# Optimization experiments

Hardware: AMD Instinct MI355X
Metric: run time of the kernel (lower is better)

Reference implementation:

```python
import jax, jax.numpy as jnp
from jax import lax
import numpy as np

DN = ('NCHW', 'OIHW', 'NCHW')

def conv2d_same(x, w, b):
    # 5x5, stride 1, pad 2 == SAME
    y = lax.conv_general_dilated(x, w, (1, 1), 'SAME', dimension_numbers=DN)
    return y + b[None, :, None, None]

def setup_inputs() -> dict:
    key = jax.random.key(0)
    ks = jax.random.split(key, 5)
    B, S, D = 8, 2048, 1024
    k55 = 0.2  # ~1/sqrt(25) init scale
    return {
        'x':  jax.random.normal(ks[0], (B, S, D), dtype=jnp.float32),
        'w1': jax.random.normal(ks[1], (1, 1, 5, 5), dtype=jnp.float32) * k55,
        'b1': jnp.zeros((1,), jnp.float32),
        'w2': jax.random.normal(ks[2], (1, 1, 5, 5), dtype=jnp.float32) * k55,
        'b2': jnp.zeros((1,), jnp.float32),
        'w3': jax.random.normal(ks[3], (1, 2, 5, 5), dtype=jnp.float32) * k55,
        'b3': jnp.zeros((1,), jnp.float32),
        'w4': jax.random.normal(ks[4], (1, 1, 5, 5), dtype=jnp.float32) * k55,
        'b4': jnp.zeros((1,), jnp.float32),
    }

def reference(x, w1, b1, w2, b2, w3, b3, w4, b4):
    # x: [b, s, d]
    xT = jnp.swapaxes(x, 1, 2)                              # [b, d, s]
    # self-similarity, softmax over BATCH dim (dim=0, as in original)
    NSSM = jax.nn.softmax(jnp.einsum('bsd,btd->bst', x, x), axis=0)   # [b, s, s]
    conv_x  = conv2d_same(x[:, None],  w1, b1)[:, 0]        # [b, s, d]
    conv_xT = conv2d_same(xT[:, None], w2, b2)[:, 0]        # [b, d, s]
    Attention_map = jax.nn.softmax(jnp.matmul(conv_x, conv_xT), axis=0)  # [b, s, s]
    Moca_map = conv2d_same(jnp.stack([NSSM, Attention_map], axis=1), w3, b3)[:, 0]  # [b, s, s]
    conv_g = conv2d_same(x[:, None], w4, b4)[:, 0]          # [b, s, d]
    Wz = jnp.matmul(Moca_map, conv_g)                       # [b, s, d]
    return Wz + x
```

## Files before the change

### kernel.cpp

```cpp
#include <hip/hip_runtime.h>

#define Bz 8
#define Sz 2048
#define Dz 1024

typedef __attribute__((ext_vector_type(8))) _Float16 f16x8;
typedef __attribute__((ext_vector_type(8))) short short8v;
typedef __attribute__((ext_vector_type(4))) short short4v;
typedef __attribute__((ext_vector_type(4))) float f32x4;

__device__ __forceinline__ short f2h(float f) {
    _Float16 h = (_Float16)f;
    return __builtin_bit_cast(short, h);
}
__device__ __forceinline__ float h2f(short s) {
    return (float)__builtin_bit_cast(_Float16, s);
}
__device__ __forceinline__ void gld16(const void* g, void* l) {
    __builtin_amdgcn_global_load_lds(
        (const __attribute__((address_space(1))) void*)g,
        (__attribute__((address_space(3))) void*)l, 16, 0, 0);
}

__global__ __launch_bounds__(256) void conv3_kernel(
    const float* __restrict__ x,
    const float* __restrict__ w1, const float* __restrict__ b1,
    const float* __restrict__ w2, const float* __restrict__ b2,
    short* __restrict__ x16, short* __restrict__ C1f, short* __restrict__ C2f)
{
    __shared__ float w[50];
    __shared__ float bias[2];
    const size_t SD = (size_t)Sz * Dz;
    int tid = threadIdx.x;
    if (tid < 25) w[tid] = w1[tid];
    else if (tid < 50) w[tid] = w2[tid - 25];
    if (tid == 50) { bias[0] = b1[0]; bias[1] = b2[0]; }
    __syncthreads();

    int d4 = tid * 4;
    int y = blockIdx.y;
    int s = ((y & 7) << 8) | (y >> 3);
    int b = blockIdx.z;
    const float* xb = x + (size_t)b * SD + d4;

    float wv[5][12];
#pragma unroll
    for (int i = 0; i < 5; i++) {
        int ss = s + i - 2;
        int ssc = ss < 0 ? 0 : (ss >= Sz ? Sz - 1 : ss);
        const float* rp = xb + (size_t)ssc * Dz;
        if (d4 > 0) *(float4*)&wv[i][0] = *(const float4*)(rp - 4);
        else { wv[i][0] = wv[i][1] = wv[i][2] = wv[i][3] = 0.f; }
        *(float4*)&wv[i][4] = *(const float4*)rp;
        if (d4 < 1020) *(float4*)&wv[i][8] = *(const float4*)(rp + 4);
        else { wv[i][8] = wv[i][9] = wv[i][10] = wv[i][11] = 0.f; }
        if (ss != ssc) {
#pragma unroll
            for (int q = 0; q < 12; q++) wv[i][q] = 0.f;
        }
    }

    float o1[4] = {}, o2[4] = {};
#pragma unroll
    for (int i = 0; i < 5; i++)
#pragma unroll
        for (int j = 0; j < 5; j++) {
            float c1w = w[i * 5 + j], c2w = w[25 + j * 5 + i];
#pragma unroll
            for (int q = 0; q < 4; q++) {
                float v = wv[i][q + j + 2];
                o1[q] = fmaf(c1w, v, o1[q]);
                o2[q] = fmaf(c2w, v, o2[q]);
            }
        }
    size_t o = (size_t)b * SD + (size_t)s * Dz + d4;
    short4v hx, h1, h2;
#pragma unroll
    for (int q = 0; q < 4; q++) {
        hx[q] = f2h(wv[2][q + 4]);
        h1[q] = f2h(o1[q] + bias[0]);
        h2[q] = f2h(o2[q] + bias[1]);
    }
    *(short4v*)(x16 + o) = hx;
    *(short4v*)(C1f + o) = h1;
    *(short4v*)(C2f + o) = h2;
}

__global__ __launch_bounds__(256) void convT_kernel(
    const float* __restrict__ x, const float* __restrict__ w4,
    const float* __restrict__ b4, short* __restrict__ C4T)
{
    __shared__ float xs[68][73];
    __shared__ short ct[64][72];
    __shared__ float w[25];
    __shared__ float bb;
    const size_t SD = (size_t)Sz * Dz;
    int tid = threadIdx.x;
    if (tid < 25) w[tid] = w4[tid];
    if (tid == 25) bb = b4[0];

    int s0 = blockIdx.x * 64, d0 = blockIdx.y * 64, b = blockIdx.z;
    const float* xb = x + (size_t)b * SD;
    for (int k = tid; k < 68 * 68; k += 256) {
        int r = k / 68, c = k - r * 68;
        int gr = s0 - 2 + r, gc = d0 - 2 + c;
        float v = 0.f;
        if (gr >= 0 && gr < Sz && gc >= 0 && gc < Dz) v = xb[(size_t)gr * Dz + gc];
        xs[r][c] = v;
    }
    __syncthreads();

    int sl = tid & 63, dg = tid >> 6;
    float acc[16];
#pragma unroll
    for (int q = 0; q < 16; q++) acc[q] = bb;
#pragma unroll
    for (int i = 0; i < 5; i++) {
        float row[20];
#pragma unroll
        for (int m = 0; m < 20; m++) row[m] = xs[sl + i][dg * 16 + m];
#pragma unroll
        for (int j = 0; j < 5; j++) {
            float wv = w[i * 5 + j];
#pragma unroll
            for (int q = 0; q < 16; q++) acc[q] = fmaf(wv, row[q + j], acc[q]);
        }
    }
#pragma unroll
    for (int q = 0; q < 16; q++) ct[dg * 16 + q][sl] = f2h(acc[q]);
    __syncthreads();

    int dl = tid >> 2, sc = (tid & 3) * 16;
    f16x8 v0 = *(const f16x8*)&ct[dl][sc];
    f16x8 v1 = *(const f16x8*)&ct[dl][sc + 8];
    short* op = C4T + (size_t)b * SD + (size_t)(d0 + dl) * Sz + s0 + sc;
    *(f16x8*)op = v0;
    *(f16x8*)(op + 8) = v1;
}

__global__ __launch_bounds__(512, 2) void logit8_f16(
    const short* __restrict__ Ag, const short* __restrict__ Bg,
    const short* __restrict__ Aa, const short* __restrict__ Ba,
    short* __restrict__ Qg, short* __restrict__ Qa,
    int rlo, int sq256off, long PS)
{
    __shared__ char lds[131072];

    int flat = blockIdx.x + 8 * (blockIdx.y + 4 * blockIdx.z);
    int nid = (flat & 7) * 64 + (flat >> 3);
    int bx = nid & 7, by = (nid >> 3) & 3, bz = nid >> 5;
    const int map = bz >> 3, bzb = bz & 7;
    if (map == 0) {
        int ntl = bx - sq256off;
        if (ntl >= 0 && ntl < 4 && ntl < by) return;
    }

    const size_t SD = (size_t)Sz * Dz;
    const int K = Dz;
    const short* A = (map ? Aa : Ag) + (size_t)bzb * SD;
    const short* B = (map ? Ba : Bg) + (size_t)bzb * SD;
    short* Q = (map ? Qa : Qg) + (size_t)bzb * PS;

    const int m0 = by * 256, n0 = bx * 256;
    const int t = threadIdx.x;
    const int lane = t & 63;
    const int w = t >> 6;
    const int wm = w >> 2, wn = w & 3;
    const int fr = lane & 15;
    const int kb = lane >> 4;

    const int cc16 = ((t & 7) ^ ((t >> 3) & 7)) * 16;
    const int tr = t >> 3;
    const int bdst = (t >> 8) * 8192 + ((t >> 3) & 31) * 128 + (t & 7) * 16;

    auto STA = [&](int tile, int h) {
        char* base = lds + (tile & 1) * 65536;
#pragma unroll
        for (int j = 0; j < 2; j++) {
            int row = m0 + j * 128 + h * 64 + tr;
            gld16((const char*)A + ((size_t)row * K + tile * 64) * 2 + cc16,
                  base + j * 16384 + h * 8192 + t * 16);
        }
    };
    auto STB = [&](int tile, int h) {
        char* base = lds + (tile & 1) * 65536 + 32768;
#pragma unroll
        for (int j = 0; j < 2; j++) {
            int u = j * 64 + tr;
            int row = n0 + (u >> 5) * 64 + h * 32 + (u & 31);
            gld16((const char*)B + ((size_t)row * K + tile * 64) * 2 + cc16,
                  base + j * 16384 + h * 4096 + bdst);
        }
    };

    int aoff[2], boff[2];
#pragma unroll
    for (int ks = 0; ks < 2; ks++) {
        int slot = ((ks * 4 + kb) ^ (fr & 7)) * 16;
        aoff[ks] = (wm * 128 + fr) * 128 + slot;
        boff[ks] = (wn * 64 + fr) * 128 + slot;
    }

    f16x8 aR[8];
    f16x8 bR[2][4];
    f32x4 acc[8][4];
#pragma unroll
    for (int i = 0; i < 8; i++)
#pragma unroll
        for (int j = 0; j < 4; j++) acc[i][j] = (f32x4){0.f, 0.f, 0.f, 0.f};

    auto LDA = [&](int qa, int d) {
        const char* p = lds + d * 65536 + qa * 8192;
#pragma unroll
        for (int f = 0; f < 4; f++)
#pragma unroll
            for (int ks = 0; ks < 2; ks++)
                aR[f * 2 + ks] = *(const f16x8*)(p + aoff[ks] + f * 2048);
    };
    auto LDB = [&](int qb, int d, int which) {
        const char* p = lds + d * 65536 + 32768 + qb * 4096;
#pragma unroll
        for (int g = 0; g < 2; g++)
#pragma unroll
            for (int ks = 0; ks < 2; ks++)
                bR[which][g * 2 + ks] = *(const f16x8*)(p + boff[ks] + g * 2048);
    };
#define MMQ(qa, qb, which)                                                        \
    __builtin_amdgcn_s_setprio(1);                                                \
    _Pragma("unroll") for (int f = 0; f < 4; f++)                                 \
        _Pragma("unroll") for (int g = 0; g < 2; g++)                             \
            _Pragma("unroll") for (int ks = 0; ks < 2; ks++)                      \
                acc[(qa)*4 + f][(qb)*2 + g] = __builtin_amdgcn_mfma_f32_16x16x32_f16( \
                    aR[f * 2 + ks], bR[which][g * 2 + ks], acc[(qa)*4 + f][(qb)*2 + g], 0, 0, 0); \
    __builtin_amdgcn_s_setprio(0);

#define BAR()  __builtin_amdgcn_s_barrier(); __builtin_amdgcn_sched_barrier(0)
#define WAIT4() asm volatile("s_waitcnt vmcnt(4)" ::: "memory"); __builtin_amdgcn_sched_barrier(0)
#define WAIT0() asm volatile("s_waitcnt vmcnt(0)" ::: "memory"); __builtin_amdgcn_sched_barrier(0)

    STA(0, 0); STB(0, 0); STA(0, 1); STB(0, 1);
    STA(1, 0); STB(1, 0);

    const int NIT = K / 128;
    for (int it = 0; it < NIT - 1; ++it) {
        const int V = 2 * it + 1, W = 2 * it + 2, X = 2 * it + 3;
        WAIT4(); BAR();
        STA(V, 1); LDA(0, 0); LDB(0, 0, 0); MMQ(0, 0, 0);
        BAR();
        STB(V, 1); LDB(1, 0, 1); MMQ(0, 1, 1);
        BAR();
        STA(W, 0); LDA(1, 0); MMQ(1, 0, 0);
        BAR();
        STB(W, 0); MMQ(1, 1, 1);
        WAIT4(); BAR();
        STA(W, 1); LDA(0, 1); LDB(0, 1, 0); MMQ(0, 0, 0);
        BAR();
        STB(W, 1); LDB(1, 1, 1); MMQ(0, 1, 1);
        BAR();
        STA(X, 0); LDA(1, 1); MMQ(1, 0, 0);
        BAR();
        STB(X, 0); MMQ(1, 1, 1);
    }
    {
        const int V = 2 * NIT - 1;
        WAIT4(); BAR();
        STA(V, 1); LDA(0, 0); LDB(0, 0, 0); MMQ(0, 0, 0);
        BAR();
        STB(V, 1); LDB(1, 0, 1); MMQ(0, 1, 1);
        BAR();
        LDA(1, 0); MMQ(1, 0, 0);
        BAR();
        MMQ(1, 1, 1);
        WAIT0(); BAR();
        LDA(0, 1); LDB(0, 1, 0); MMQ(0, 0, 0);
        BAR();
        LDB(1, 1, 1); MMQ(0, 1, 1);
        BAR();
        LDA(1, 1); MMQ(1, 0, 0);
        BAR();
        MMQ(1, 1, 1);
    }
#undef MMQ
#undef BAR
#undef WAIT4
#undef WAIT0

#pragma unroll
    for (int mf = 0; mf < 8; mf++)
#pragma unroll
        for (int nf = 0; nf < 4; nf++) {
            int col = n0 + wn * 64 + nf * 16 + fr;
#pragma unroll
            for (int r = 0; r < 4; r++) {
                int rowg = m0 + wm * 128 + mf * 16 + kb * 4 + r;
                float o = acc[mf][nf][r];
                if (map == 0 && rlo + rowg == col) o -= 1024.f;
                Q[(size_t)rowg * Sz + col] = f2h(o);
            }
        }
}

__global__ __launch_bounds__(512, 2) void wz8_f16(
    const short* __restrict__ M0, const short* __restrict__ M1,
    const short* __restrict__ C4Tm,
    const float* __restrict__ X, float* __restrict__ Out,
    long psM0, long psM1)
{
    __shared__ char lds[131072];

    int flat = blockIdx.x + 4 * (blockIdx.y + 8 * blockIdx.z);
    int nid = (flat & 7) * 32 + (flat >> 3);
    int bx = nid & 3, by = (nid >> 2) & 7, bz = nid >> 5;

    const size_t SD = (size_t)Sz * Dz;
    const int K = Sz;
    const short* A0 = M0 + (size_t)bz * psM0;
    const short* A1 = M1 + (size_t)bz * psM1;
    const short* B = C4Tm + (size_t)bz * SD;
    const float* Src = X + (size_t)bz * SD;
    float* C = Out + (size_t)bz * SD;

    const int m0 = by * 256, n0 = bx * 256;
    const int t = threadIdx.x;
    const int lane = t & 63;
    const int w = t >> 6;
    const int wm = w >> 2, wn = w & 3;
    const int fr = lane & 15;
    const int kb = lane >> 4;

    const int cc16 = ((t & 7) ^ ((t >> 3) & 7)) * 16;
    const int tr = t >> 3;
    const int bdst = (t >> 8) * 8192 + ((t >> 3) & 31) * 128 + (t & 7) * 16;

    auto STA = [&](int tile, int h) {
        char* base = lds + (tile & 1) * 65536;
#pragma unroll
        for (int j = 0; j < 2; j++) {
            int row = m0 + j * 128 + h * 64 + tr;
            const short* src = (row < 1022) ? (A0 + (size_t)row * K)
                                            : (A1 + (size_t)(row - 1022) * K);
            gld16((const char*)src + (size_t)tile * 128 + cc16,
                  base + j * 16384 + h * 8192 + t * 16);
        }
    };
    auto STB = [&](int tile, int h) {
        char* base = lds + (tile & 1) * 65536 + 32768;
#pragma unroll
        for (int j = 0; j < 2; j++) {
            int u = j * 64 + tr;
            int row = n0 + (u >> 5) * 64 + h * 32 + (u & 31);
            gld16((const char*)B + ((size_t)row * K + tile * 64) * 2 + cc16,
                  base + j * 16384 + h * 4096 + bdst);
        }
    };

    int aoff[2], boff[2];
#pragma unroll
    for (int ks = 0; ks < 2; ks++) {
        int slot = ((ks * 4 + kb) ^ (fr & 7)) * 16;
        aoff[ks] = (wm * 128 + fr) * 128 + slot;
        boff[ks] = (wn * 64 + fr) * 128 + slot;
    }

    f16x8 aR[8];
    f16x8 bR[2][4];
    f32x4 acc[8][4];
#pragma unroll
    for (int i = 0; i < 8; i++)
#pragma unroll
        for (int j = 0; j < 4; j++) acc[i][j] = (f32x4){0.f, 0.f, 0.f, 0.f};

    auto LDA = [&](int qa, int d) {
        const char* p = lds + d * 65536 + qa * 8192;
#pragma unroll
        for (int f = 0; f < 4; f++)
#pragma unroll
            for (int ks = 0; ks < 2; ks++)
                aR[f * 2 + ks] = *(const f16x8*)(p + aoff[ks] + f * 2048);
    };
    auto LDB = [&](int qb, int d, int which) {
        const char* p = lds + d * 65536 + 32768 + qb * 4096;
#pragma unroll
        for (int g = 0; g < 2; g++)
#pragma unroll
            for (int ks = 0; ks < 2; ks++)
                bR[which][g * 2 + ks] = *(const f16x8*)(p + boff[ks] + g * 2048);
    };
#define MMQ(qa, qb, which)                                                        \
    __builtin_amdgcn_s_setprio(1);                                                \
    _Pragma("unroll") for (int f = 0; f < 4; f++)                                 \
        _Pragma("unroll") for (int g = 0; g < 2; g++)                             \
            _Pragma("unroll") for (int ks = 0; ks < 2; ks++)                      \
                acc[(qa)*4 + f][(qb)*2 + g] = __builtin_amdgcn_mfma_f32_16x16x32_f16( \
                    aR[f * 2 + ks], bR[which][g * 2 + ks], acc[(qa)*4 + f][(qb)*2 + g], 0, 0, 0); \
    __builtin_amdgcn_s_setprio(0);

#define BAR()  __builtin_amdgcn_s_barrier(); __builtin_amdgcn_sched_barrier(0)
#define WAIT4() asm volatile("s_waitcnt vmcnt(4)" ::: "memory"); __builtin_amdgcn_sched_barrier(0)
#define WAIT0() asm volatile("s_waitcnt vmcnt(0)" ::: "memory"); __builtin_amdgcn_sched_barrier(0)

    STA(0, 0); STB(0, 0); STA(0, 1); STB(0, 1);
    STA(1, 0); STB(1, 0);

    const int NIT = K / 128;
    for (int it = 0; it < NIT - 1; ++it) {
        const int V = 2 * it + 1, W = 2 * it + 2, X2 = 2 * it + 3;
        WAIT4(); BAR();
        STA(V, 1); LDA(0, 0); LDB(0, 0, 0); MMQ(0, 0, 0);
        BAR();
        STB(V, 1); LDB(1, 0, 1); MMQ(0, 1, 1);
        BAR();
        STA(W, 0); LDA(1, 0); MMQ(1, 0, 0);
        BAR();
        STB(W, 0); MMQ(1, 1, 1);
        WAIT4(); BAR();
        STA(W, 1); LDA(0, 1); LDB(0, 1, 0); MMQ(0, 0, 0);
        BAR();
        STB(W, 1); LDB(1, 1, 1); MMQ(0, 1, 1);
        BAR();
        STA(X2, 0); LDA(1, 1); MMQ(1, 0, 0);
        BAR();
        STB(X2, 0); MMQ(1, 1, 1);
    }
    {
        const int V = 2 * NIT - 1;
        WAIT4(); BAR();
        STA(V, 1); LDA(0, 0); LDB(0, 0, 0); MMQ(0, 0, 0);
        BAR();
        STB(V, 1); LDB(1, 0, 1); MMQ(0, 1, 1);
        BAR();
        LDA(1, 0); MMQ(1, 0, 0);
        BAR();
        MMQ(1, 1, 1);
        WAIT0(); BAR();
        LDA(0, 1); LDB(0, 1, 0); MMQ(0, 0, 0);
        BAR();
        LDB(1, 1, 1); MMQ(0, 1, 1);
        BAR();
        LDA(1, 1); MMQ(1, 0, 0);
        BAR();
        MMQ(1, 1, 1);
    }
#undef MMQ
#undef BAR
#undef WAIT4
#undef WAIT0

#pragma unroll
    for (int mf = 0; mf < 8; mf++)
#pragma unroll
        for (int nf = 0; nf < 4; nf++) {
            int col = n0 + wn * 64 + nf * 16 + fr;
#pragma unroll
            for (int r = 0; r < 4; r++) {
                int rowg = m0 + wm * 128 + mf * 16 + kb * 4 + r;
                C[(size_t)rowg * Dz + col] = acc[mf][nf][r] + Src[(size_t)rowg * Dz + col];
            }
        }
}

__global__ __launch_bounds__(256) void mirror_g(
    short* __restrict__ F, int o0, long PS)
{
    __shared__ short ts[128][136];
    int p = blockIdx.x, b = blockIdx.y;
    int mi = 1, base = 0;
    while (p >= base + mi) { base += mi; mi++; }
    int nt = p - base;
    short* Fb = F + (size_t)b * PS;
    int t = threadIdx.x;
    int rr = t >> 1, c0 = (t & 1) * 64;
    const short* src = Fb + (size_t)(nt * 128 + rr) * Sz + o0 + mi * 128 + c0;
#pragma unroll
    for (int j = 0; j < 8; j++)
        *(short8v*)&ts[rr][c0 + j * 8] = *(const short8v*)(src + j * 8);
    __syncthreads();
    short* dst = Fb + (size_t)(mi * 128 + rr) * Sz + o0 + nt * 128 + c0;
#pragma unroll
    for (int j = 0; j < 8; j++) {
        short8v v;
#pragma unroll
        for (int e = 0; e < 8; e++) v[e] = ts[c0 + j * 8 + e][rr];
        *(short8v*)(dst + j * 8) = v;
    }
}

__global__ __launch_bounds__(256) void softmax_ip(
    short* __restrict__ Qg, short* __restrict__ Qa, int nElem, long ps)
{
    int i8 = (blockIdx.x * 256 + threadIdx.x) * 8;
    if (i8 >= nElem) return;
    short* Q = blockIdx.z ? Qa : Qg;

    short8v v[Bz];
    float f[Bz][8];
#pragma unroll
    for (int b = 0; b < Bz; b++) {
        v[b] = *(const short8v*)(Q + i8 + (size_t)b * ps);
#pragma unroll
        for (int e = 0; e < 8; e++) f[b][e] = h2f(v[b][e]);
    }
#pragma unroll
    for (int e = 0; e < 8; e++) {
        float mx = f[0][e];
#pragma unroll
        for (int b = 1; b < Bz; b++) mx = fmaxf(mx, f[b][e]);
        float sum = 0.f;
#pragma unroll
        for (int b = 0; b < Bz; b++) { f[b][e] = __expf(f[b][e] - mx); sum += f[b][e]; }
        float inv = 1.f / sum;
#pragma unroll
        for (int b = 0; b < Bz; b++) v[b][e] = f2h(f[b][e] * inv);
    }
#pragma unroll
    for (int b = 0; b < Bz; b++)
        *(short8v*)(Q + i8 + (size_t)b * ps) = v[b];
}

__global__ __launch_bounds__(256) void slab_copy(
    const short* __restrict__ Fg, const short* __restrict__ Fa,
    short* __restrict__ slab, long PS)
{
    int idx = blockIdx.x * 256 + threadIdx.x;
    int e = idx * 8;
    int map = e >> 16;
    int rem = e & 65535;
    int b = rem >> 13;
    int rem2 = rem & 8191;
    int row = rem2 >> 11;
    int col = rem2 & 2047;
    const short* src = (map ? Fa : Fg) + (size_t)b * PS + (size_t)(1020 + row) * Sz + col;
    *(short8v*)(slab + e) = *(const short8v*)src;
}

__global__ __launch_bounds__(256) void moca_kernel(
    const short* __restrict__ Gs, const short* __restrict__ As,
    const short* __restrict__ slab,
    const float* __restrict__ w3, const float* __restrict__ b3,
    short* __restrict__ Mout,
    int o0, int rlo, int slabLo, long psIn, long psOut)
{
    __shared__ float w[50];
    __shared__ float bb;
    int tid = threadIdx.x;
    if (tid < 50) w[tid] = w3[tid];
    if (tid == 50) bb = b3[0];
    __syncthreads();

    int t8 = tid * 8;
    int so = blockIdx.y, b = blockIdx.z;
    int s = o0 + so;
    const short* Gp = Gs + (size_t)b * psIn;
    const short* Ap = As + (size_t)b * psIn;

    float acc[8];
#pragma unroll
    for (int q = 0; q < 8; q++) acc[q] = bb;

#pragma unroll
    for (int i = 0; i < 5; i++) {
        int sr = s + i - 2;
        if (sr < 0 || sr >= Sz) continue;
        const short *gp, *ap;
        size_t ro;
        if (sr >= rlo) { gp = Gp; ap = Ap; ro = (size_t)(sr - rlo) * Sz; }
        else {
            gp = slab + (size_t)b * 8192;
            ap = slab + 65536 + (size_t)b * 8192;
            ro = (size_t)(sr - slabLo) * Sz;
        }
        float gw[16], aw[16];
#pragma unroll
        for (int g = 0; g < 4; g++) {
            int c0 = t8 - 4 + g * 4;
            if (c0 >= 0 && c0 + 3 < Sz) {
                short4v gv = *(const short4v*)(gp + ro + c0);
                short4v av = *(const short4v*)(ap + ro + c0);
#pragma unroll
                for (int e = 0; e < 4; e++) { gw[g * 4 + e] = h2f(gv[e]); aw[g * 4 + e] = h2f(av[e]); }
            } else {
#pragma unroll
                for (int e = 0; e < 4; e++) { gw[g * 4 + e] = 0.f; aw[g * 4 + e] = 0.f; }
            }
        }
#pragma unroll
        for (int j = 0; j < 5; j++) {
            float wg = w[i * 5 + j], wa = w[25 + i * 5 + j];
#pragma unroll
            for (int q = 0; q < 8; q++)
                acc[q] = fmaf(wg, gw[q + j + 2], fmaf(wa, aw[q + j + 2], acc[q]));
        }
    }
    short4v r0, r1;
#pragma unroll
    for (int q = 0; q < 4; q++) { r0[q] = f2h(acc[q]); r1[q] = f2h(acc[q + 4]); }
    short* op = Mout + (size_t)b * psOut + (size_t)so * Sz + t8;
    *(short4v*)op = r0;
    *(short4v*)(op + 4) = r1;
}

extern "C" void kernel_launch(void* const* d_in, const int* in_sizes, int n_in,
                              void* d_out, int out_size, void* d_ws, size_t ws_size,
                              hipStream_t stream)
{
    const float* x  = (const float*)d_in[0];
    const float* w1 = (const float*)d_in[1];
    const float* b1 = (const float*)d_in[2];
    const float* w2 = (const float*)d_in[3];
    const float* b2 = (const float*)d_in[4];
    const float* w3 = (const float*)d_in[5];
    const float* b3 = (const float*)d_in[6];
    const float* w4 = (const float*)d_in[7];
    const float* b4 = (const float*)d_in[8];
    float* out = (float*)d_out;

    const size_t SD = (size_t)Sz * Dz;
    const size_t BSD2 = (size_t)Bz * SD * 2;

    char* ws = (char*)d_ws;
    short* x16 = (short*)(ws);
    short* C1f = (short*)(ws + 1 * BSD2);
    short* C2f = (short*)(ws + 2 * BSD2);
    short* C4T = (short*)(ws + 3 * BSD2);
    char* strip0 = ws + 4 * BSD2;

    const size_t PS   = (size_t)1024 * Sz;
    const size_t PSM0 = (size_t)1022 * Sz;
    const size_t PSM1 = (size_t)1026 * Sz;
    short* Fg   = (short*)strip0;
    short* Fa   = Fg + (size_t)Bz * PS;
    short* Mf0  = Fa + (size_t)Bz * PS;
    short* slab = Mf0 + (size_t)Bz * PSM0;
    short* Mf1  = x16;

    conv3_kernel<<<dim3(1, Sz, Bz), 256, 0, stream>>>(
        x, w1, b1, w2, b2, x16, C1f, C2f);
    convT_kernel<<<dim3(Sz / 64, Dz / 64, Bz), 256, 0, stream>>>(x, w4, b4, C4T);

    const int ne = 1024 * Sz;

    logit8_f16<<<dim3(8, 4, 16), 512, 0, stream>>>(
        x16, x16, C1f, C2f, Fg, Fa, 0, 0, (long)PS);
    mirror_g<<<dim3(28, Bz), 256, 0, stream>>>(Fg, 0, (long)PS);
    softmax_ip<<<dim3((ne / 8 + 255) / 256, 1, 2), 256, 0, stream>>>(Fg, Fa, ne, (long)PS);
    slab_copy<<<dim3(64), 256, 0, stream>>>(Fg, Fa, slab, (long)PS);
    moca_kernel<<<dim3(1, 1022, Bz), 256, 0, stream>>>(
        Fg, Fa, slab, w3, b3, Mf0, 0, 0, 0, (long)PS, (long)PSM0);

    logit8_f16<<<dim3(8, 4, 16), 512, 0, stream>>>(
        x16 + (size_t)1024 * Dz, x16, C1f + (size_t)1024 * Dz, C2f,
        Fg, Fa, 1024, 4, (long)PS);
    mirror_g<<<dim3(28, Bz), 256, 0, stream>>>(Fg, 1024, (long)PS);
    softmax_ip<<<dim3((ne / 8 + 255) / 256, 1, 2), 256, 0, stream>>>(Fg, Fa, ne, (long)PS);
    moca_kernel<<<dim3(1, 1026, Bz), 256, 0, stream>>>(
        Fg, Fa, slab, w3, b3, Mf1, 1022, 1024, 1020, (long)PS, (long)PSM1);

    wz8_f16<<<dim3(4, 8, 8), 512, 0, stream>>>(
        Mf0, Mf1, C4T, x, out, (long)PSM0, (long)PSM1);
}
```

Before: 505.7 us.

## Switch GEMMs to 32x32x16 MFMA and fuse slab copy into softmax

New measurement: 528.6 us. 4.5% more time.

```diff
diff --git a/kernel.cpp b/kernel.cpp
--- a/kernel.cpp
+++ b/kernel.cpp
@@ -7,7 +7,7 @@
 typedef __attribute__((ext_vector_type(8))) _Float16 f16x8;
 typedef __attribute__((ext_vector_type(8))) short short8v;
 typedef __attribute__((ext_vector_type(4))) short short4v;
-typedef __attribute__((ext_vector_type(4))) float f32x4;
+typedef __attribute__((ext_vector_type(16))) float f32x16;
 
 __device__ __forceinline__ short f2h(float f) {
     _Float16 h = (_Float16)f;
@@ -166,8 +166,7 @@
     const int lane = t & 63;
     const int w = t >> 6;
     const int wm = w >> 2, wn = w & 3;
-    const int fr = lane & 15;
-    const int kb = lane >> 4;
+    const int l31 = lane & 31, l5 = lane >> 5, l7 = lane & 7;
 
     const int cc16 = ((t & 7) ^ ((t >> 3) & 7)) * 16;
     const int tr = t >> 3;
@@ -193,45 +192,42 @@
         }
     };
 
-    int aoff[2], boff[2];
-#pragma unroll
-    for (int ks = 0; ks < 2; ks++) {
-        int slot = ((ks * 4 + kb) ^ (fr & 7)) * 16;
-        aoff[ks] = (wm * 128 + fr) * 128 + slot;
-        boff[ks] = (wn * 64 + fr) * 128 + slot;
-    }
-
-    f16x8 aR[8];
+    int aoff[4], boff[4];
+#pragma unroll
+    for (int ks = 0; ks < 4; ks++) {
+        int slot = ((ks * 2 + l5) ^ l7) * 16;
+        aoff[ks] = (wm * 128 + l31) * 128 + slot;
+        boff[ks] = (wn * 64 + l31) * 128 + slot;
+    }
+
+    f16x8 aR[2][4];
     f16x8 bR[2][4];
-    f32x4 acc[8][4];
-#pragma unroll
-    for (int i = 0; i < 8; i++)
-#pragma unroll
-        for (int j = 0; j < 4; j++) acc[i][j] = (f32x4){0.f, 0.f, 0.f, 0.f};
+    f32x16 acc[4][2];
+#pragma unroll
+    for (int i = 0; i < 4; i++)
+#pragma unroll
+        for (int j = 0; j < 2; j++) acc[i][j] = (f32x16)(0.f);
 
     auto LDA = [&](int qa, int d) {
         const char* p = lds + d * 65536 + qa * 8192;
 #pragma unroll
-        for (int f = 0; f < 4; f++)
-#pragma unroll
-            for (int ks = 0; ks < 2; ks++)
-                aR[f * 2 + ks] = *(const f16x8*)(p + aoff[ks] + f * 2048);
+        for (int i = 0; i < 2; i++)
+#pragma unroll
+            for (int ks = 0; ks < 4; ks++)
+                aR[i][ks] = *(const f16x8*)(p + i * 4096 + aoff[ks]);
     };
     auto LDB = [&](int qb, int d, int which) {
         const char* p = lds + d * 65536 + 32768 + qb * 4096;
 #pragma unroll
-        for (int g = 0; g < 2; g++)
-#pragma unroll
-            for (int ks = 0; ks < 2; ks++)
-                bR[which][g * 2 + ks] = *(const f16x8*)(p + boff[ks] + g * 2048);
+        for (int ks = 0; ks < 4; ks++)
+            bR[which][ks] = *(const f16x8*)(p + boff[ks]);
     };
 #define MMQ(qa, qb, which)                                                        \
     __builtin_amdgcn_s_setprio(1);                                                \
-    _Pragma("unroll") for (int f = 0; f < 4; f++)                                 \
-        _Pragma("unroll") for (int g = 0; g < 2; g++)                             \
-            _Pragma("unroll") for (int ks = 0; ks < 2; ks++)                      \
-                acc[(qa)*4 + f][(qb)*2 + g] = __builtin_amdgcn_mfma_f32_16x16x32_f16( \
-                    aR[f * 2 + ks], bR[which][g * 2 + ks], acc[(qa)*4 + f][(qb)*2 + g], 0, 0, 0); \
+    _Pragma("unroll") for (int i = 0; i < 2; i++)                                 \
+        _Pragma("unroll") for (int ks = 0; ks < 4; ks++)                          \
+            acc[(qa)*2 + i][qb] = __builtin_amdgcn_mfma_f32_32x32x16_f16(         \
+                aR[i][ks], bR[which][ks], acc[(qa)*2 + i][qb], 0, 0, 0);          \
     __builtin_amdgcn_s_setprio(0);
 
 #define BAR()  __builtin_amdgcn_s_barrier(); __builtin_amdgcn_sched_barrier(0)
@@ -286,14 +282,14 @@
 #undef WAIT0
 
 #pragma unroll
-    for (int mf = 0; mf < 8; mf++)
-#pragma unroll
-        for (int nf = 0; nf < 4; nf++) {
-            int col = n0 + wn * 64 + nf * 16 + fr;
-#pragma unroll
-            for (int r = 0; r < 4; r++) {
-                int rowg = m0 + wm * 128 + mf * 16 + kb * 4 + r;
-                float o = acc[mf][nf][r];
+    for (int fa = 0; fa < 4; fa++)
+#pragma unroll
+        for (int fb = 0; fb < 2; fb++) {
+            int col = n0 + wn * 64 + fb * 32 + l31;
+#pragma unroll
+            for (int r = 0; r < 16; r++) {
+                int rowg = m0 + wm * 128 + fa * 32 + (r & 3) + 8 * (r >> 2) + 4 * l5;
+                float o = acc[fa][fb][r];
                 if (map == 0 && rlo + rowg == col) o -= 1024.f;
                 Q[(size_t)rowg * Sz + col] = f2h(o);
             }
@@ -325,8 +321,7 @@
     const int lane = t & 63;
     const int w = t >> 6;
     const int wm = w >> 2, wn = w & 3;
-    const int fr = lane & 15;
-    const int kb = lane >> 4;
+    const int l31 = lane & 31, l5 = lane >> 5, l7 = lane & 7;
 
     const int cc16 = ((t & 7) ^ ((t >> 3) & 7)) * 16;
     const int tr = t >> 3;
@@ -354,45 +349,42 @@
         }
     };
 
-    int aoff[2], boff[2];
-#pragma unroll
-    for (int ks = 0; ks < 2; ks++) {
-        int slot = ((ks * 4 + kb) ^ (fr & 7)) * 16;
-        aoff[ks] = (wm * 128 + fr) * 128 + slot;
-        boff[ks] = (wn * 64 + fr) * 128 + slot;
-    }
-
-    f16x8 aR[8];
+    int aoff[4], boff[4];
+#pragma unroll
+    for (int ks = 0; ks < 4; ks++) {
+        int slot = ((ks * 2 + l5) ^ l7) * 16;
+        aoff[ks] = (wm * 128 + l31) * 128 + slot;
+        boff[ks] = (wn * 64 + l31) * 128 + slot;
+    }
+
+    f16x8 aR[2][4];
     f16x8 bR[2][4];
-    f32x4 acc[8][4];
-#pragma unroll
-    for (int i = 0; i < 8; i++)
-#pragma unroll
-        for (int j = 0; j < 4; j++) acc[i][j] = (f32x4){0.f, 0.f, 0.f, 0.f};
+    f32x16 acc[4][2];
+#pragma unroll
+    for (int i = 0; i < 4; i++)
+#pragma unroll
+        for (int j = 0; j < 2; j++) acc[i][j] = (f32x16)(0.f);
 
     auto LDA = [&](int qa, int d) {
         const char* p = lds + d * 65536 + qa * 8192;
 #pragma unroll
-        for (int f = 0; f < 4; f++)
-#pragma unroll
-            for (int ks = 0; ks < 2; ks++)
-                aR[f * 2 + ks] = *(const f16x8*)(p + aoff[ks] + f * 2048);
+        for (int i = 0; i < 2; i++)
+#pragma unroll
+            for (int ks = 0; ks < 4; ks++)
+                aR[i][ks] = *(const f16x8*)(p + i * 4096 + aoff[ks]);
     };
     auto LDB = [&](int qb, int d, int which) {
         const char* p = lds + d * 65536 + 32768 + qb * 4096;
 #pragma unroll
-        for (int g = 0; g < 2; g++)
-#pragma unroll
-            for (int ks = 0; ks < 2; ks++)
-                bR[which][g * 2 + ks] = *(const f16x8*)(p + boff[ks] + g * 2048);
+        for (int ks = 0; ks < 4; ks++)
+            bR[which][ks] = *(const f16x8*)(p + boff[ks]);
     };
 #define MMQ(qa, qb, which)                                                        \
     __builtin_amdgcn_s_setprio(1);                                                \
-    _Pragma("unroll") for (int f = 0; f < 4; f++)                                 \
-        _Pragma("unroll") for (int g = 0; g < 2; g++)                             \
-            _Pragma("unroll") for (int ks = 0; ks < 2; ks++)                      \
-                acc[(qa)*4 + f][(qb)*2 + g] = __builtin_amdgcn_mfma_f32_16x16x32_f16( \
-                    aR[f * 2 + ks], bR[which][g * 2 + ks], acc[(qa)*4 + f][(qb)*2 + g], 0, 0, 0); \
+    _Pragma("unroll") for (int i = 0; i < 2; i++)                                 \
+        _Pragma("unroll") for (int ks = 0; ks < 4; ks++)                          \
+            acc[(qa)*2 + i][qb] = __builtin_amdgcn_mfma_f32_32x32x16_f16(         \
+                aR[i][ks], bR[which][ks], acc[(qa)*2 + i][qb], 0, 0, 0);          \
     __builtin_amdgcn_s_setprio(0);
 
 #define BAR()  __builtin_amdgcn_s_barrier(); __builtin_amdgcn_sched_barrier(0)
@@ -447,14 +439,14 @@
 #undef WAIT0
 
 #pragma unroll
-    for (int mf = 0; mf < 8; mf++)
-#pragma unroll
-        for (int nf = 0; nf < 4; nf++) {
-            int col = n0 + wn * 64 + nf * 16 + fr;
-#pragma unroll
-            for (int r = 0; r < 4; r++) {
-                int rowg = m0 + wm * 128 + mf * 16 + kb * 4 + r;
-                C[(size_t)rowg * Dz + col] = acc[mf][nf][r] + Src[(size_t)rowg * Dz + col];
+    for (int fa = 0; fa < 4; fa++)
+#pragma unroll
+        for (int fb = 0; fb < 2; fb++) {
+            int col = n0 + wn * 64 + fb * 32 + l31;
+#pragma unroll
+            for (int r = 0; r < 16; r++) {
+                int rowg = m0 + wm * 128 + fa * 32 + (r & 3) + 8 * (r >> 2) + 4 * l5;
+                C[(size_t)rowg * Dz + col] = acc[fa][fb][r] + Src[(size_t)rowg * Dz + col];
             }
         }
 }
@@ -486,11 +478,13 @@
 }
 
 __global__ __launch_bounds__(256) void softmax_ip(
-    short* __restrict__ Qg, short* __restrict__ Qa, int nElem, long ps)
+    short* __restrict__ Qg, short* __restrict__ Qa,
+    short* __restrict__ slab, int writeSlab, int nElem, long ps)
 {
     int i8 = (blockIdx.x * 256 + threadIdx.x) * 8;
     if (i8 >= nElem) return;
-    short* Q = blockIdx.z ? Qa : Qg;
+    int z = blockIdx.z;
+    short* Q = z ? Qa : Qg;
 
     short8v v[Bz];
     float f[Bz][8];
@@ -515,22 +509,15 @@
 #pragma unroll
     for (int b = 0; b < Bz; b++)
         *(short8v*)(Q + i8 + (size_t)b * ps) = v[b];
-}
-
-__global__ __launch_bounds__(256) void slab_copy(
-    const short* __restrict__ Fg, const short* __restrict__ Fa,
-    short* __restrict__ slab, long PS)
-{
-    int idx = blockIdx.x * 256 + threadIdx.x;
-    int e = idx * 8;
-    int map = e >> 16;
-    int rem = e & 65535;
-    int b = rem >> 13;
-    int rem2 = rem & 8191;
-    int row = rem2 >> 11;
-    int col = rem2 & 2047;
-    const short* src = (map ? Fa : Fg) + (size_t)b * PS + (size_t)(1020 + row) * Sz + col;
-    *(short8v*)(slab + e) = *(const short8v*)src;
+
+    int row = i8 >> 11;
+    if (writeSlab && row >= 1020 && row < 1024) {
+        int col = i8 & 2047;
+        int roff = z * 65536 + (row - 1020) * 2048 + col;
+#pragma unroll
+        for (int b = 0; b < Bz; b++)
+            *(short8v*)(slab + roff + b * 8192) = v[b];
+    }
 }
 
 __global__ __launch_bounds__(256) void moca_kernel(
@@ -642,8 +629,8 @@
     logit8_f16<<<dim3(8, 4, 16), 512, 0, stream>>>(
         x16, x16, C1f, C2f, Fg, Fa, 0, 0, (long)PS);
     mirror_g<<<dim3(28, Bz), 256, 0, stream>>>(Fg, 0, (long)PS);
-    softmax_ip<<<dim3((ne / 8 + 255) / 256, 1, 2), 256, 0, stream>>>(Fg, Fa, ne, (long)PS);
-    slab_copy<<<dim3(64), 256, 0, stream>>>(Fg, Fa, slab, (long)PS);
+    softmax_ip<<<dim3((ne / 8 + 255) / 256, 1, 2), 256, 0, stream>>>(
+        Fg, Fa, slab, 1, ne, (long)PS);
     moca_kernel<<<dim3(1, 1022, Bz), 256, 0, stream>>>(
         Fg, Fa, slab, w3, b3, Mf0, 0, 0, 0, (long)PS, (long)PSM0);
 
@@ -651,7 +638,8 @@
         x16 + (size_t)1024 * Dz, x16, C1f + (size_t)1024 * Dz, C2f,
         Fg, Fa, 1024, 4, (long)PS);
     mirror_g<<<dim3(28, Bz), 256, 0, stream>>>(Fg, 1024, (long)PS);
-    softmax_ip<<<dim3((ne / 8 + 255) / 256, 1, 2), 256, 0, stream>>>(Fg, Fa, ne, (long)PS);
+    softmax_ip<<<dim3((ne / 8 + 255) / 256, 1, 2), 256, 0, stream>>>(
+        Fg, Fa, slab, 0, ne, (long)PS);
     moca_kernel<<<dim3(1, 1026, Bz), 256, 0, stream>>>(
         Fg, Fa, slab, w3, b3, Mf1, 1022, 1024, 1020, (long)PS, (long)PSM1);
 
```
